# Optimization experiments

Hardware: AMD Instinct MI355X
Metric: run time of the kernel (lower is better)

The kernel has to match this reference:

```python
import math
import jax, jax.numpy as jnp
import numpy as np

B, S, H, NH = 2, 2048, 1024, 16
HD = H // NH


def setup_inputs() -> dict:
    key = jax.random.key(0)
    k1, k2, k3 = jax.random.split(key, 3)
    scale = 1.0 / math.sqrt(H)
    return {
        "hidden_states": jax.random.normal(k1, (B, S, H), dtype=jnp.float32),
        "attention_mask": jnp.ones((B, 1, S, S), dtype=jnp.float32),
        "qkv_w": jax.random.normal(k2, (3 * H, H), dtype=jnp.float32) * scale,
        "qkv_b": jnp.zeros((3 * H,), dtype=jnp.float32),
        "dense_w": jax.random.normal(k3, (H, H), dtype=jnp.float32) * scale,
        "dense_b": jnp.zeros((H,), dtype=jnp.float32),
    }


def reference(hidden_states, attention_mask, qkv_w, qkv_b, dense_w, dense_b):
    # qkv projection: torch Linear y = x @ W^T + b
    mixed = hidden_states @ qkv_w.T + qkv_b            # [B,S,3H]
    mixed = mixed.reshape(B, S, NH, 3 * HD).transpose(0, 2, 1, 3)  # [B,NH,S,3HD]
    q, k, v = jnp.split(mixed, 3, axis=-1)             # each [B,NH,S,HD]
    scores = jnp.einsum("bhqd,bhkd->bhqk", q, k) / math.sqrt(HD)
    scores = scores * attention_mask - 10000.0 * (1.0 - attention_mask)
    probs = jax.nn.softmax(scores, axis=-1)            # dropout p=0 -> identity
    ctx = jnp.einsum("bhqk,bhkd->bhqd", probs, v)      # [B,NH,S,HD]
    ctx = ctx.transpose(0, 2, 1, 3).reshape(B, S, H)
    out = ctx @ dense_w.T + dense_b                    # output dropout p=0
    return out
```

## Files before the change

### kernel.cpp

```cpp
#include <hip/hip_runtime.h>
#include <hip/hip_bf16.h>
#include <stdint.h>

#define BB 2
#define SS 2048
#define HH 1024
#define NHH 16
#define HDD 64
#define MM (BB*SS)
#define N1 (3*HH)
#define NT (SS/64)
#define LOG2E 1.44269504f

using bf16 = __hip_bfloat16;
typedef __attribute__((ext_vector_type(8))) short bf16x8;
typedef __attribute__((ext_vector_type(4))) float f32x4;

__device__ inline unsigned short f2bfu(float f) {
  union { bf16 h; unsigned short u; } c;
  c.h = __float2bfloat16(f);
  return c.u;
}

__device__ inline unsigned int cvtpk(float lo, float hi) {
  unsigned int r;
  asm("v_cvt_pk_bf16_f32 %0, %1, %2" : "=v"(r) : "v"(lo), "v"(hi));
  return r;
}

__device__ inline void load_lds16(const void* g, void* l) {
  __builtin_amdgcn_global_load_lds(
      (const __attribute__((address_space(1))) void*)g,
      (__attribute__((address_space(3))) void*)l, 16, 0, 0);
}

__device__ inline f32x4 mfma16(bf16x8 a, bf16x8 b, f32x4 c) {
  return __builtin_amdgcn_mfma_f32_16x16x32_bf16(a, b, c, 0, 0, 0);
}

__global__ __launch_bounds__(256) void prep_kernel(const float* __restrict__ mask,
                                                   unsigned char* __restrict__ flags,
                                                   const float* __restrict__ a,
                                                   unsigned short* __restrict__ ao, int na4,
                                                   const float* __restrict__ bsrc,
                                                   unsigned short* __restrict__ bo, int nb4,
                                                   const float* __restrict__ c,
                                                   unsigned short* __restrict__ co, int nc4) {
  if (blockIdx.x < 2048) {
    int t = blockIdx.x;
    int b = t >> 10, qt = (t >> 5) & 31, kt = t & 31;
    const float* mb = mask + ((size_t)b * SS + qt * 64) * SS + kt * 64;
    int row = threadIdx.x >> 2, c0 = (threadIdx.x & 3) * 16;
    int ok = 1;
#pragma unroll
    for (int j = 0; j < 4; ++j) {
      float4 v = *reinterpret_cast<const float4*>(mb + (size_t)row * SS + c0 + j * 4);
      ok &= (v.x == 1.f) & (v.y == 1.f) & (v.z == 1.f) & (v.w == 1.f);
    }
    ok = __all(ok);
    __shared__ int s[4];
    if ((threadIdx.x & 63) == 0) s[threadIdx.x >> 6] = ok;
    __syncthreads();
    if (threadIdx.x == 0) flags[t] = (unsigned char)(s[0] & s[1] & s[2] & s[3]);
    return;
  }
  int total = na4 + nb4 + nc4;
  int nblk = gridDim.x - 2048;
  int st = nblk * blockDim.x;
  for (int i = (blockIdx.x - 2048) * blockDim.x + threadIdx.x; i < total; i += st) {
    const float* in; unsigned short* out; int j = i;
    if (j < na4) { in = a; out = ao; }
    else if (j < na4 + nb4) { j -= na4; in = bsrc; out = bo; }
    else { j -= na4 + nb4; in = c; out = co; }
    float4 v = reinterpret_cast<const float4*>(in)[j];
    ushort4 o;
    o.x = f2bfu(v.x); o.y = f2bfu(v.y); o.z = f2bfu(v.z); o.w = f2bfu(v.w);
    reinterpret_cast<ushort4*>(out)[j] = o;
  }
}

__global__ __launch_bounds__(256) void vtrans_kernel(const unsigned short* __restrict__ mixed,
                                                     unsigned short* __restrict__ vT) {
  __shared__ unsigned short t[64 * 72];
  const int st = blockIdx.x, bh = blockIdx.y;
  const int b = bh >> 4, h = bh & 15;
  const int r = threadIdx.x >> 2, c0 = (threadIdx.x & 3) * 16;

  const unsigned short* src = mixed + ((size_t)(b * SS) + st * 64) * N1 + h * 192 + 128;
  union { bf16x8 v; unsigned short u[8]; } A, B;
  A.v = *reinterpret_cast<const bf16x8*>(src + (size_t)r * N1 + c0);
  B.v = *reinterpret_cast<const bf16x8*>(src + (size_t)r * N1 + c0 + 8);
#pragma unroll
  for (int j = 0; j < 8; ++j) t[(c0 + j) * 72 + r] = A.u[j];
#pragma unroll
  for (int j = 0; j < 8; ++j) t[(c0 + 8 + j) * 72 + r] = B.u[j];
  __syncthreads();

  unsigned short* dst = vT + ((size_t)bh * HDD + r) * SS + st * 64 + c0;
  bf16x8 o0 = *reinterpret_cast<const bf16x8*>(&t[r * 72 + c0]);
  bf16x8 o1 = *reinterpret_cast<const bf16x8*>(&t[r * 72 + c0 + 8]);
  *reinterpret_cast<bf16x8*>(dst) = o0;
  *reinterpret_cast<bf16x8*>(dst + 8) = o1;
}

template <bool OUT_BF16>
__global__ __launch_bounds__(256) void gemm_bt(const unsigned short* __restrict__ A,
                                               const unsigned short* __restrict__ Bt,
                                               const float* __restrict__ bias,
                                               void* __restrict__ Cv,
                                               int Ndim, int Kdim) {
  __shared__ __align__(16) unsigned short As[128 * 64];
  __shared__ __align__(16) unsigned short Bs[128 * 64];

  const int tid = threadIdx.x;
  const int wave = tid >> 6, lane = tid & 63;
  const int m0 = blockIdx.x * 128;
  const int n0 = blockIdx.y * 128;
  const int wm = (wave >> 1) * 64, wn = (wave & 1) * 64;
  const int lrow = lane & 15;
  const int g = lane >> 4;
  const int r4 = (lane >> 4) * 4;
  const int x0 = (g ^ (lrow & 7)) << 3;
  const int x1 = ((g + 4) ^ (lrow & 7)) << 3;

  f32x4 acc[4][4];
  const f32x4 z = {0.f, 0.f, 0.f, 0.f};
  for (int i = 0; i < 4; ++i)
    for (int j = 0; j < 4; ++j) acc[i][j] = z;

  for (int k0 = 0; k0 < Kdim; k0 += 64) {
#pragma unroll
    for (int it = 0; it < 4; ++it) {
      int idx = it * 256 + tid;
      int row = idx >> 3, seg = idx & 7;
      int sw = (seg ^ (row & 7)) << 3;
      load_lds16(A + (size_t)(m0 + row) * Kdim + k0 + sw, &As[row * 64 + seg * 8]);
      load_lds16(Bt + (size_t)(n0 + row) * Kdim + k0 + sw, &Bs[row * 64 + seg * 8]);
    }
    __syncthreads();

    bf16x8 af[4], bfr[4];
#pragma unroll
    for (int i = 0; i < 4; ++i)
      af[i] = *reinterpret_cast<const bf16x8*>(&As[(wm + i * 16 + lrow) * 64 + x0]);
#pragma unroll
    for (int j = 0; j < 4; ++j)
      bfr[j] = *reinterpret_cast<const bf16x8*>(&Bs[(wn + j * 16 + lrow) * 64 + x0]);
#pragma unroll
    for (int i = 0; i < 4; ++i)
#pragma unroll
      for (int j = 0; j < 4; ++j)
        acc[i][j] = mfma16(af[i], bfr[j], acc[i][j]);
#pragma unroll
    for (int i = 0; i < 4; ++i)
      af[i] = *reinterpret_cast<const bf16x8*>(&As[(wm + i * 16 + lrow) * 64 + x1]);
#pragma unroll
    for (int j = 0; j < 4; ++j)
      bfr[j] = *reinterpret_cast<const bf16x8*>(&Bs[(wn + j * 16 + lrow) * 64 + x1]);
#pragma unroll
    for (int i = 0; i < 4; ++i)
#pragma unroll
      for (int j = 0; j < 4; ++j)
        acc[i][j] = mfma16(af[i], bfr[j], acc[i][j]);
    __syncthreads();
  }

#pragma unroll
  for (int i = 0; i < 4; ++i) {
#pragma unroll
    for (int j = 0; j < 4; ++j) {
      int col = n0 + wn + j * 16 + lrow;
      float bv = bias[col];
#pragma unroll
      for (int r = 0; r < 4; ++r) {
        int row = m0 + wm + i * 16 + r4 + r;
        float v = acc[i][j][r] + bv;
        if (OUT_BF16) {
          ((unsigned short*)Cv)[(size_t)row * Ndim + col] = f2bfu(v);
        } else {
          ((float*)Cv)[(size_t)row * Ndim + col] = v;
        }
      }
    }
  }
}

__global__ __launch_bounds__(256, 4) void attn_kernel(const unsigned short* __restrict__ mixed,
                                                      const unsigned short* __restrict__ vT,
                                                      const float* __restrict__ mask,
                                                      const unsigned char* __restrict__ flags,
                                                      unsigned short* __restrict__ ctx) {
  __shared__ __align__(16) unsigned short Ks[2][64 * 64];
  __shared__ __align__(16) unsigned short Vt[2][64 * 64];
  __shared__ __align__(16) unsigned short QP[64 * 64];

  const int tid = threadIdx.x, wave = tid >> 6, lane = tid & 63;
  const int ql = lane & 15;
  const int g = lane >> 4;
  const int q0 = blockIdx.x * 64;
  const int bh = blockIdx.y;
  const int b = bh / NHH, hh = bh % NHH;

  const unsigned short* qbase = mixed + (size_t)(b * SS) * N1 + hh * 192;
  const unsigned short* kbase = qbase + 64;
  const unsigned short* vtbase = vT + ((size_t)(b * NHH + hh) * HDD) * SS;
  const float* mbase = mask + (size_t)b * SS * SS;
  const unsigned char* fl = flags + ((size_t)b * 32 + blockIdx.x) * 32;

  const int srow = tid >> 3, sseg = tid & 7;
  const int swst = (sseg ^ (srow & 7)) << 3;

  load_lds16(qbase + (size_t)(q0 + srow) * N1 + swst, &QP[srow * 64 + sseg * 8]);
  load_lds16(qbase + (size_t)(q0 + 32 + srow) * N1 + swst, &QP[(32 + srow) * 64 + sseg * 8]);
  load_lds16(kbase + (size_t)srow * N1 + swst, &Ks[0][srow * 64 + sseg * 8]);
  load_lds16(kbase + (size_t)(32 + srow) * N1 + swst, &Ks[0][(32 + srow) * 64 + sseg * 8]);
  load_lds16(vtbase + (size_t)srow * SS + swst, &Vt[0][srow * 64 + sseg * 8]);
  load_lds16(vtbase + (size_t)(32 + srow) * SS + swst, &Vt[0][(32 + srow) * 64 + sseg * 8]);
  __syncthreads();

  const int qrow = wave * 16 + ql;
  const bf16x8 qf0 = *reinterpret_cast<const bf16x8*>(
      &QP[qrow * 64 + ((g ^ (qrow & 7)) << 3)]);
  const bf16x8 qf1 = *reinterpret_cast<const bf16x8*>(
      &QP[qrow * 64 + (((g + 4) ^ (qrow & 7)) << 3)]);
  __syncthreads();

  const int s0 = (g ^ (ql & 7)) << 3;
  const int s1 = ((g + 4) ^ (ql & 7)) << 3;
  const unsigned short* KrA = &Ks[0][ql * 64 + s0];
  const unsigned short* KrB = &Ks[0][ql * 64 + s1];
  const unsigned short* VrA = &Vt[0][ql * 64 + s0];
  const unsigned short* VrB = &Vt[0][ql * 64 + s1];
  unsigned short* Ps = &QP[wave * 1024];
  const int X = (ql & 7) << 3;
  unsigned short* Pw0 = &Ps[ql * 64 + ((4 * g) ^ X)];
  unsigned short* Pw1 = &Ps[ql * 64 + ((16 + 4 * g) ^ X)];
  unsigned short* Pw2 = &Ps[ql * 64 + ((32 + 4 * g) ^ X)];
  unsigned short* Pw3 = &Ps[ql * 64 + ((48 + 4 * g) ^ X)];
  const unsigned short* Pr0 = &Ps[ql * 64 + ((8 * g) ^ X)];
  const unsigned short* Pr1 = &Ps[ql * 64 + ((32 + 8 * g) ^ X)];

  const unsigned short* kpre = kbase + (size_t)(64 + srow) * N1 + swst;
  const unsigned short* vpre = vtbase + (size_t)srow * SS + 64 + swst;

  f32x4 oacc[4];
  const f32x4 z = {0.f, 0.f, 0.f, 0.f};
  for (int fd = 0; fd < 4; ++fd) oacc[fd] = z;
  float lsum = 0.f;
  const float C2 = 0.125f * LOG2E;

#define TILE_BODY(CUR_, KT_, HAVENEXT_)                                         \
  {                                                                             \
    const int kt_ = (KT_);                                                      \
    if (HAVENEXT_) {                                                            \
      load_lds16(kpre, &Ks[(CUR_)^1][srow * 64 + sseg * 8]);                    \
      load_lds16(kpre + 32 * N1, &Ks[(CUR_)^1][(32 + srow) * 64 + sseg * 8]);   \
      load_lds16(vpre, &Vt[(CUR_)^1][srow * 64 + sseg * 8]);                    \
      load_lds16(vpre + 32 * SS, &Vt[(CUR_)^1][(32 + srow) * 64 + sseg * 8]);   \
    }                                                                           \
    kpre += 64 * N1; vpre += 64;                                                \
    f32x4 sacc[4];                                                              \
    __builtin_amdgcn_s_setprio(1);                                              \
    _Pragma("unroll")                                                           \
    for (int n = 0; n < 4; ++n) {                                               \
      bf16x8 k0 = *reinterpret_cast<const bf16x8*>(KrA + (CUR_)*4096 + n*1024); \
      bf16x8 k1 = *reinterpret_cast<const bf16x8*>(KrB + (CUR_)*4096 + n*1024); \
      sacc[n] = mfma16(k0, qf0, z);                                             \
      sacc[n] = mfma16(k1, qf1, sacc[n]);                                       \
    }                                                                           \
    __builtin_amdgcn_s_setprio(0);                                              \
              \
    bf16x8 bv00 = *reinterpret_cast<const bf16x8*>(VrA + (CUR_)*4096 + 0*1024); \
    bf16x8 bv10 = *reinterpret_cast<const bf16x8*>(VrB + (CUR_)*4096 + 0*1024); \
    bf16x8 bv01 = *reinterpret_cast<const bf16x8*>(VrA + (CUR_)*4096 + 1*1024); \
    bf16x8 bv11 = *reinterpret_cast<const bf16x8*>(VrB + (CUR_)*4096 + 1*1024); \
    bf16x8 bv02 = *reinterpret_cast<const bf16x8*>(VrA + (CUR_)*4096 + 2*1024); \
    bf16x8 bv12 = *reinterpret_cast<const bf16x8*>(VrB + (CUR_)*4096 + 2*1024); \
    bf16x8 bv03 = *reinterpret_cast<const bf16x8*>(VrA + (CUR_)*4096 + 3*1024); \
    bf16x8 bv13 = *reinterpret_cast<const bf16x8*>(VrB + (CUR_)*4096 + 3*1024); \
    const bool allones = fl[kt_] != 0;                                          \
    float pv[4][4];                                                             \
    if (allones) {                                                              \
      _Pragma("unroll")                                                         \
      for (int n = 0; n < 4; ++n)                                               \
        _Pragma("unroll")                                                       \
        for (int r = 0; r < 4; ++r)                                             \
          pv[n][r] = exp2f(sacc[n][r] * C2);                                    \
    } else {                                                                    \
      int qq = q0 + wave * 16 + ql;                                             \
      _Pragma("unroll")                                                         \
      for (int n = 0; n < 4; ++n)                                               \
        _Pragma("unroll")                                                       \
        for (int r = 0; r < 4; ++r) {                                           \
          int kk = kt_ * 64 + 16 * n + 4 * g + r;                               \
          float mv = mbase[(size_t)qq * SS + kk];                               \
          float s = sacc[n][r] * 0.125f;                                        \
          pv[n][r] = exp2f((s * mv - 10000.f * (1.f - mv)) * LOG2E);            \
        }                                                                       \
    }                                                                           \
    { uint2 w; w.x = cvtpk(pv[0][0], pv[0][1]); w.y = cvtpk(pv[0][2], pv[0][3]);\
      *reinterpret_cast<uint2*>(Pw0) = w; }                                     \
    { uint2 w; w.x = cvtpk(pv[1][0], pv[1][1]); w.y = cvtpk(pv[1][2], pv[1][3]);\
      *reinterpret_cast<uint2*>(Pw1) = w; }                                     \
    { uint2 w; w.x = cvtpk(pv[2][0], pv[2][1]); w.y = cvtpk(pv[2][2], pv[2][3]);\
      *reinterpret_cast<uint2*>(Pw2) = w; }                                     \
    { uint2 w; w.x = cvtpk(pv[3][0], pv[3][1]); w.y = cvtpk(pv[3][2], pv[3][3]);\
      *reinterpret_cast<uint2*>(Pw3) = w; }                                     \
                    \
    {                                                                           \
      float t00 = (pv[0][0] + pv[0][1]) + (pv[0][2] + pv[0][3]);                \
      float t01 = (pv[1][0] + pv[1][1]) + (pv[1][2] + pv[1][3]);                \
      float t10 = (pv[2][0] + pv[2][1]) + (pv[2][2] + pv[2][3]);                \
      float t11 = (pv[3][0] + pv[3][1]) + (pv[3][2] + pv[3][3]);                \
      lsum += (t00 + t01) + (t10 + t11);                                        \
    }                                                                           \
    bf16x8 pa0 = *reinterpret_cast<const bf16x8*>(Pr0);                         \
    bf16x8 pa1 = *reinterpret_cast<const bf16x8*>(Pr1);                         \
    __builtin_amdgcn_s_setprio(1);                                              \
    oacc[0] = mfma16(pa0, bv00, oacc[0]);                                       \
    oacc[1] = mfma16(pa0, bv01, oacc[1]);                                       \
    oacc[2] = mfma16(pa0, bv02, oacc[2]);                                       \
    oacc[3] = mfma16(pa0, bv03, oacc[3]);                                       \
    oacc[0] = mfma16(pa1, bv10, oacc[0]);                                       \
    oacc[1] = mfma16(pa1, bv11, oacc[1]);                                       \
    oacc[2] = mfma16(pa1, bv12, oacc[2]);                                       \
    oacc[3] = mfma16(pa1, bv13, oacc[3]);                                       \
    __builtin_amdgcn_s_setprio(0);                                              \
    __syncthreads();                                                            \
  }

  for (int kt = 0; kt < NT; kt += 2) {
    TILE_BODY(0, kt, true)
    TILE_BODY(1, kt + 1, (kt + 2 < NT))
  }
#undef TILE_BODY

  float lrun = lsum;
  lrun += __shfl_xor(lrun, 16, 64);
  lrun += __shfl_xor(lrun, 32, 64);
  float invl = 1.f / lrun;
#pragma unroll
  for (int r = 0; r < 4; ++r) {
    float inv = __shfl(invl, g * 4 + r, 64);
    int qq = q0 + wave * 16 + g * 4 + r;
    unsigned short* cp = ctx + (size_t)(b * SS + qq) * HH + hh * HDD;
#pragma unroll
    for (int fd = 0; fd < 4; ++fd)
      cp[fd * 16 + ql] = f2bfu(oacc[fd][r] * inv);
  }
}

extern "C" void kernel_launch(void* const* d_in, const int* in_sizes, int n_in,
                              void* d_out, int out_size, void* d_ws, size_t ws_size,
                              hipStream_t stream) {
  const float* hs      = (const float*)d_in[0];
  const float* mask    = (const float*)d_in[1];
  const float* qkv_w   = (const float*)d_in[2];
  const float* qkv_b   = (const float*)d_in[3];
  const float* dense_w = (const float*)d_in[4];
  const float* dense_b = (const float*)d_in[5];
  float* out = (float*)d_out;

  char* ws = (char*)d_ws;
  unsigned short* hs_b     = (unsigned short*)(ws);
  unsigned short* qkvw_b   = (unsigned short*)(ws + 8388608);
  unsigned short* densew_b = (unsigned short*)(ws + 14680064);
  unsigned short* mixed_b  = (unsigned short*)(ws + 16777216);
  unsigned short* ctx_b    = (unsigned short*)(ws + 41943040);
  unsigned char*  flags    = (unsigned char*)(ws + 50331648);
  unsigned short* vT_b     = (unsigned short*)(ws + 50335744);

  prep_kernel<<<4096, 256, 0, stream>>>(mask, flags,
                                        hs, hs_b, (MM * HH) / 4,
                                        qkv_w, qkvw_b, (N1 * HH) / 4,
                                        dense_w, densew_b, (HH * HH) / 4);

  gemm_bt<true><<<dim3(MM / 128, N1 / 128), 256, 0, stream>>>(
      hs_b, qkvw_b, qkv_b, mixed_b, N1, HH);

  vtrans_kernel<<<dim3(SS / 64, BB * NHH), 256, 0, stream>>>(mixed_b, vT_b);

  attn_kernel<<<dim3(SS / 64, BB * NHH), 256, 0, stream>>>(
      mixed_b, vT_b, mask, flags, ctx_b);

  gemm_bt<false><<<dim3(MM / 128, HH / 128), 256, 0, stream>>>(
      ctx_b, densew_b, dense_b, out, HH, HH);
}
```

Before: 146.8 us.

## Split KV tiles across wave pairs with 32-row waves and LDS merge

Each wave now handles 32 query rows instead of 16. Each K and V fragment read from LDS therefore feeds two MFMA chains, which halves LDS fragment traffic per FLOP. The two wave pairs alternate over KV tiles: one pair computes while the next tile is staged. At the end, pair 1's partial outputs and row sums go through LDS and are added into pair 0's results before normalization. In exchange, register pressure roughly doubles, only half the waves in a block compute at any moment, and a final reduction step is added.

```diff
diff --git a/kernel.cpp b/kernel.cpp
--- a/kernel.cpp
+++ b/kernel.cpp
@@ -197,6 +197,8 @@
   const int tid = threadIdx.x, wave = tid >> 6, lane = tid & 63;
   const int ql = lane & 15;
   const int g = lane >> 4;
+  const int pair = wave >> 1;
+  const int rb = (wave & 1) * 32;
   const int q0 = blockIdx.x * 64;
   const int bh = blockIdx.y;
   const int b = bh / NHH, hh = bh % NHH;
@@ -218,11 +220,11 @@
   load_lds16(vtbase + (size_t)(32 + srow) * SS + swst, &Vt[0][(32 + srow) * 64 + sseg * 8]);
   __syncthreads();
 
-  const int qrow = wave * 16 + ql;
-  const bf16x8 qf0 = *reinterpret_cast<const bf16x8*>(
-      &QP[qrow * 64 + ((g ^ (qrow & 7)) << 3)]);
-  const bf16x8 qf1 = *reinterpret_cast<const bf16x8*>(
-      &QP[qrow * 64 + (((g + 4) ^ (qrow & 7)) << 3)]);
+  const int qrA = rb + ql, qrB = rb + 16 + ql;
+  const bf16x8 qfA0 = *reinterpret_cast<const bf16x8*>(&QP[qrA * 64 + ((g ^ (qrA & 7)) << 3)]);
+  const bf16x8 qfA1 = *reinterpret_cast<const bf16x8*>(&QP[qrA * 64 + (((g + 4) ^ (qrA & 7)) << 3)]);
+  const bf16x8 qfB0 = *reinterpret_cast<const bf16x8*>(&QP[qrB * 64 + ((g ^ (qrB & 7)) << 3)]);
+  const bf16x8 qfB1 = *reinterpret_cast<const bf16x8*>(&QP[qrB * 64 + (((g + 4) ^ (qrB & 7)) << 3)]);
   __syncthreads();
 
   const int s0 = (g ^ (ql & 7)) << 3;
@@ -243,110 +245,167 @@
   const unsigned short* kpre = kbase + (size_t)(64 + srow) * N1 + swst;
   const unsigned short* vpre = vtbase + (size_t)srow * SS + 64 + swst;
 
-  f32x4 oacc[4];
+  f32x4 oaccA[4], oaccB[4];
   const f32x4 z = {0.f, 0.f, 0.f, 0.f};
-  for (int fd = 0; fd < 4; ++fd) oacc[fd] = z;
-  float lsum = 0.f;
+  for (int fd = 0; fd < 4; ++fd) { oaccA[fd] = z; oaccB[fd] = z; }
+  float lsumA = 0.f, lsumB = 0.f;
   const float C2 = 0.125f * LOG2E;
 
-#define TILE_BODY(CUR_, KT_, HAVENEXT_)                                         \
+#define STAGE(NXT_)                                                             \
+  {                                                                             \
+    load_lds16(kpre, &Ks[NXT_][srow * 64 + sseg * 8]);                          \
+    load_lds16(kpre + 32 * N1, &Ks[NXT_][(32 + srow) * 64 + sseg * 8]);         \
+    load_lds16(vpre, &Vt[NXT_][srow * 64 + sseg * 8]);                          \
+    load_lds16(vpre + 32 * SS, &Vt[NXT_][(32 + srow) * 64 + sseg * 8]);         \
+    kpre += 64 * N1; vpre += 64;                                                \
+  }
+
+#define COMPUTE(CUR_, KT_)                                                      \
   {                                                                             \
     const int kt_ = (KT_);                                                      \
-    if (HAVENEXT_) {                                                            \
-      load_lds16(kpre, &Ks[(CUR_)^1][srow * 64 + sseg * 8]);                    \
-      load_lds16(kpre + 32 * N1, &Ks[(CUR_)^1][(32 + srow) * 64 + sseg * 8]);   \
-      load_lds16(vpre, &Vt[(CUR_)^1][srow * 64 + sseg * 8]);                    \
-      load_lds16(vpre + 32 * SS, &Vt[(CUR_)^1][(32 + srow) * 64 + sseg * 8]);   \
-    }                                                                           \
-    kpre += 64 * N1; vpre += 64;                                                \
-    f32x4 sacc[4];                                                              \
+    f32x4 saccA[4], saccB[4];                                                   \
     __builtin_amdgcn_s_setprio(1);                                              \
     _Pragma("unroll")                                                           \
     for (int n = 0; n < 4; ++n) {                                               \
       bf16x8 k0 = *reinterpret_cast<const bf16x8*>(KrA + (CUR_)*4096 + n*1024); \
       bf16x8 k1 = *reinterpret_cast<const bf16x8*>(KrB + (CUR_)*4096 + n*1024); \
-      sacc[n] = mfma16(k0, qf0, z);                                             \
-      sacc[n] = mfma16(k1, qf1, sacc[n]);                                       \
+      saccA[n] = mfma16(k0, qfA0, z);                                           \
+      saccA[n] = mfma16(k1, qfA1, saccA[n]);                                    \
+      saccB[n] = mfma16(k0, qfB0, z);                                           \
+      saccB[n] = mfma16(k1, qfB1, saccB[n]);                                    \
     }                                                                           \
     __builtin_amdgcn_s_setprio(0);                                              \
-              \
-    bf16x8 bv00 = *reinterpret_cast<const bf16x8*>(VrA + (CUR_)*4096 + 0*1024); \
-    bf16x8 bv10 = *reinterpret_cast<const bf16x8*>(VrB + (CUR_)*4096 + 0*1024); \
-    bf16x8 bv01 = *reinterpret_cast<const bf16x8*>(VrA + (CUR_)*4096 + 1*1024); \
-    bf16x8 bv11 = *reinterpret_cast<const bf16x8*>(VrB + (CUR_)*4096 + 1*1024); \
-    bf16x8 bv02 = *reinterpret_cast<const bf16x8*>(VrA + (CUR_)*4096 + 2*1024); \
-    bf16x8 bv12 = *reinterpret_cast<const bf16x8*>(VrB + (CUR_)*4096 + 2*1024); \
-    bf16x8 bv03 = *reinterpret_cast<const bf16x8*>(VrA + (CUR_)*4096 + 3*1024); \
-    bf16x8 bv13 = *reinterpret_cast<const bf16x8*>(VrB + (CUR_)*4096 + 3*1024); \
     const bool allones = fl[kt_] != 0;                                          \
-    float pv[4][4];                                                             \
+    float pvA[4][4], pvB[4][4];                                                 \
     if (allones) {                                                              \
       _Pragma("unroll")                                                         \
       for (int n = 0; n < 4; ++n)                                               \
         _Pragma("unroll")                                                       \
-        for (int r = 0; r < 4; ++r)                                             \
-          pv[n][r] = exp2f(sacc[n][r] * C2);                                    \
+        for (int r = 0; r < 4; ++r) {                                           \
+          pvA[n][r] = exp2f(saccA[n][r] * C2);                                  \
+          pvB[n][r] = exp2f(saccB[n][r] * C2);                                  \
+        }                                                                       \
     } else {                                                                    \
-      int qq = q0 + wave * 16 + ql;                                             \
+      int qqA = q0 + rb + ql;                                                   \
       _Pragma("unroll")                                                         \
       for (int n = 0; n < 4; ++n)                                               \
         _Pragma("unroll")                                                       \
         for (int r = 0; r < 4; ++r) {                                           \
           int kk = kt_ * 64 + 16 * n + 4 * g + r;                               \
-          float mv = mbase[(size_t)qq * SS + kk];                               \
-          float s = sacc[n][r] * 0.125f;                                        \
-          pv[n][r] = exp2f((s * mv - 10000.f * (1.f - mv)) * LOG2E);            \
+          float mvA = mbase[(size_t)qqA * SS + kk];                             \
+          float mvB = mbase[(size_t)(qqA + 16) * SS + kk];                      \
+          float sA = saccA[n][r] * 0.125f;                                      \
+          float sB = saccB[n][r] * 0.125f;                                      \
+          pvA[n][r] = exp2f((sA * mvA - 10000.f * (1.f - mvA)) * LOG2E);        \
+          pvB[n][r] = exp2f((sB * mvB - 10000.f * (1.f - mvB)) * LOG2E);        \
         }                                                                       \
     }                                                                           \
-    { uint2 w; w.x = cvtpk(pv[0][0], pv[0][1]); w.y = cvtpk(pv[0][2], pv[0][3]);\
+    {                                                                           \
+      float tA0 = (pvA[0][0] + pvA[0][1]) + (pvA[0][2] + pvA[0][3]);            \
+      float tA1 = (pvA[1][0] + pvA[1][1]) + (pvA[1][2] + pvA[1][3]);            \
+      float tA2 = (pvA[2][0] + pvA[2][1]) + (pvA[2][2] + pvA[2][3]);            \
+      float tA3 = (pvA[3][0] + pvA[3][1]) + (pvA[3][2] + pvA[3][3]);            \
+      lsumA += (tA0 + tA1) + (tA2 + tA3);                                       \
+      float tB0 = (pvB[0][0] + pvB[0][1]) + (pvB[0][2] + pvB[0][3]);            \
+      float tB1 = (pvB[1][0] + pvB[1][1]) + (pvB[1][2] + pvB[1][3]);            \
+      float tB2 = (pvB[2][0] + pvB[2][1]) + (pvB[2][2] + pvB[2][3]);            \
+      float tB3 = (pvB[3][0] + pvB[3][1]) + (pvB[3][2] + pvB[3][3]);            \
+      lsumB += (tB0 + tB1) + (tB2 + tB3);                                       \
+    }                                                                           \
+         \
+    { uint2 w; w.x = cvtpk(pvA[0][0], pvA[0][1]); w.y = cvtpk(pvA[0][2], pvA[0][3]); \
       *reinterpret_cast<uint2*>(Pw0) = w; }                                     \
-    { uint2 w; w.x = cvtpk(pv[1][0], pv[1][1]); w.y = cvtpk(pv[1][2], pv[1][3]);\
+    { uint2 w; w.x = cvtpk(pvA[1][0], pvA[1][1]); w.y = cvtpk(pvA[1][2], pvA[1][3]); \
       *reinterpret_cast<uint2*>(Pw1) = w; }                                     \
-    { uint2 w; w.x = cvtpk(pv[2][0], pv[2][1]); w.y = cvtpk(pv[2][2], pv[2][3]);\
+    { uint2 w; w.x = cvtpk(pvA[2][0], pvA[2][1]); w.y = cvtpk(pvA[2][2], pvA[2][3]); \
       *reinterpret_cast<uint2*>(Pw2) = w; }                                     \
-    { uint2 w; w.x = cvtpk(pv[3][0], pv[3][1]); w.y = cvtpk(pv[3][2], pv[3][3]);\
+    { uint2 w; w.x = cvtpk(pvA[3][0], pvA[3][1]); w.y = cvtpk(pvA[3][2], pvA[3][3]); \
       *reinterpret_cast<uint2*>(Pw3) = w; }                                     \
-                    \
-    {                                                                           \
-      float t00 = (pv[0][0] + pv[0][1]) + (pv[0][2] + pv[0][3]);                \
-      float t01 = (pv[1][0] + pv[1][1]) + (pv[1][2] + pv[1][3]);                \
-      float t10 = (pv[2][0] + pv[2][1]) + (pv[2][2] + pv[2][3]);                \
-      float t11 = (pv[3][0] + pv[3][1]) + (pv[3][2] + pv[3][3]);                \
-      lsum += (t00 + t01) + (t10 + t11);                                        \
+    bf16x8 paA0 = *reinterpret_cast<const bf16x8*>(Pr0);                        \
+    bf16x8 paA1 = *reinterpret_cast<const bf16x8*>(Pr1);                        \
+    { uint2 w; w.x = cvtpk(pvB[0][0], pvB[0][1]); w.y = cvtpk(pvB[0][2], pvB[0][3]); \
+      *reinterpret_cast<uint2*>(Pw0) = w; }                                     \
+    { uint2 w; w.x = cvtpk(pvB[1][0], pvB[1][1]); w.y = cvtpk(pvB[1][2], pvB[1][3]); \
+      *reinterpret_cast<uint2*>(Pw1) = w; }                                     \
+    { uint2 w; w.x = cvtpk(pvB[2][0], pvB[2][1]); w.y = cvtpk(pvB[2][2], pvB[2][3]); \
+      *reinterpret_cast<uint2*>(Pw2) = w; }                                     \
+    { uint2 w; w.x = cvtpk(pvB[3][0], pvB[3][1]); w.y = cvtpk(pvB[3][2], pvB[3][3]); \
+      *reinterpret_cast<uint2*>(Pw3) = w; }                                     \
+    bf16x8 paB0 = *reinterpret_cast<const bf16x8*>(Pr0);                        \
+    bf16x8 paB1 = *reinterpret_cast<const bf16x8*>(Pr1);                        \
+                        \
+    __builtin_amdgcn_s_setprio(1);                                              \
+    _Pragma("unroll")                                                           \
+    for (int fd = 0; fd < 4; ++fd) {                                            \
+      bf16x8 bv0 = *reinterpret_cast<const bf16x8*>(VrA + (CUR_)*4096 + fd*1024); \
+      bf16x8 bv1 = *reinterpret_cast<const bf16x8*>(VrB + (CUR_)*4096 + fd*1024); \
+      oaccA[fd] = mfma16(paA0, bv0, oaccA[fd]);                                 \
+      oaccA[fd] = mfma16(paA1, bv1, oaccA[fd]);                                 \
+      oaccB[fd] = mfma16(paB0, bv0, oaccB[fd]);                                 \
+      oaccB[fd] = mfma16(paB1, bv1, oaccB[fd]);                                 \
     }                                                                           \
-    bf16x8 pa0 = *reinterpret_cast<const bf16x8*>(Pr0);                         \
-    bf16x8 pa1 = *reinterpret_cast<const bf16x8*>(Pr1);                         \
-    __builtin_amdgcn_s_setprio(1);                                              \
-    oacc[0] = mfma16(pa0, bv00, oacc[0]);                                       \
-    oacc[1] = mfma16(pa0, bv01, oacc[1]);                                       \
-    oacc[2] = mfma16(pa0, bv02, oacc[2]);                                       \
-    oacc[3] = mfma16(pa0, bv03, oacc[3]);                                       \
-    oacc[0] = mfma16(pa1, bv10, oacc[0]);                                       \
-    oacc[1] = mfma16(pa1, bv11, oacc[1]);                                       \
-    oacc[2] = mfma16(pa1, bv12, oacc[2]);                                       \
-    oacc[3] = mfma16(pa1, bv13, oacc[3]);                                       \
     __builtin_amdgcn_s_setprio(0);                                              \
-    __syncthreads();                                                            \
   }
 
   for (int kt = 0; kt < NT; kt += 2) {
-    TILE_BODY(0, kt, true)
-    TILE_BODY(1, kt + 1, (kt + 2 < NT))
-  }
-#undef TILE_BODY
-
-  float lrun = lsum;
-  lrun += __shfl_xor(lrun, 16, 64);
-  lrun += __shfl_xor(lrun, 32, 64);
-  float invl = 1.f / lrun;
-#pragma unroll
-  for (int r = 0; r < 4; ++r) {
-    float inv = __shfl(invl, g * 4 + r, 64);
-    int qq = q0 + wave * 16 + g * 4 + r;
-    unsigned short* cp = ctx + (size_t)(b * SS + qq) * HH + hh * HDD;
-#pragma unroll
-    for (int fd = 0; fd < 4; ++fd)
-      cp[fd * 16 + ql] = f2bfu(oacc[fd][r] * inv);
+    STAGE(1)
+    if (pair == 0) COMPUTE(0, kt)
+    __syncthreads();
+    if (kt + 2 < NT) STAGE(0)
+    if (pair == 1) COMPUTE(1, kt + 1)
+    __syncthreads();
+  }
+#undef STAGE
+#undef COMPUTE
+
+  lsumA += __shfl_xor(lsumA, 16, 64);
+  lsumA += __shfl_xor(lsumA, 32, 64);
+  lsumB += __shfl_xor(lsumB, 16, 64);
+  lsumB += __shfl_xor(lsumB, 32, 64);
+
+  float* Osh = reinterpret_cast<float*>(&Ks[0][0]);
+  float* Lsh = reinterpret_cast<float*>(&Vt[0][0]);
+  if (pair == 1) {
+#pragma unroll
+    for (int r = 0; r < 4; ++r) {
+      int rowA = rb + g * 4 + r, rowB = rb + 16 + g * 4 + r;
+#pragma unroll
+      for (int fd = 0; fd < 4; ++fd) {
+        Osh[rowA * 64 + fd * 16 + ql] = oaccA[fd][r];
+        Osh[rowB * 64 + fd * 16 + ql] = oaccB[fd][r];
+      }
+    }
+    Lsh[rb + ql] = lsumA;
+    Lsh[rb + 16 + ql] = lsumB;
+  }
+  __syncthreads();
+  if (pair == 0) {
+#pragma unroll
+    for (int r = 0; r < 4; ++r) {
+      int rowA = rb + g * 4 + r, rowB = rb + 16 + g * 4 + r;
+#pragma unroll
+      for (int fd = 0; fd < 4; ++fd) {
+        oaccA[fd][r] += Osh[rowA * 64 + fd * 16 + ql];
+        oaccB[fd][r] += Osh[rowB * 64 + fd * 16 + ql];
+      }
+    }
+    float lA = lsumA + Lsh[rb + ql];
+    float lB = lsumB + Lsh[rb + 16 + ql];
+    float invA = 1.f / lA;
+    float invB = 1.f / lB;
+#pragma unroll
+    for (int r = 0; r < 4; ++r) {
+      float iA = __shfl(invA, g * 4 + r, 64);
+      float iB = __shfl(invB, g * 4 + r, 64);
+      int qqA = q0 + rb + g * 4 + r;
+      unsigned short* cpA = ctx + (size_t)(b * SS + qqA) * HH + hh * HDD;
+      unsigned short* cpB = ctx + (size_t)(b * SS + qqA + 16) * HH + hh * HDD;
+#pragma unroll
+      for (int fd = 0; fd < 4; ++fd) {
+        cpA[fd * 16 + ql] = f2bfu(oaccA[fd][r] * iA);
+        cpB[fd * 16 + ql] = f2bfu(oaccB[fd][r] * iB);
+      }
+    }
   }
 }
 
```

Result: slower. 184.6 us (+25.7%).

## Split QKV GEMM into QK and V GEMMs writing transposed V directly

Applied to the files above, without the earlier changes.

Replaces the single QKV projection GEMM plus separate V-transpose kernel with two GEMMs. One writes Q/K into a compact per-head buffer, and the other computes V and transposes it through shared memory into the head-major vT layout. This removes the V write and read round trip and one kernel launch. The cost is two launches with a smaller grid each, where gemm_v has only 256 blocks, which may underfill the device.

```diff
diff --git a/kernel.cpp b/kernel.cpp
--- a/kernel.cpp
+++ b/kernel.cpp
@@ -9,6 +9,7 @@
 #define HDD 64
 #define MM (BB*SS)
 #define N1 (3*HH)
+#define QKS 2048
 #define NT (SS/64)
 #define LOG2E 1.44269504f
 
@@ -79,35 +80,179 @@
   }
 }
 
-__global__ __launch_bounds__(256) void vtrans_kernel(const unsigned short* __restrict__ mixed,
-                                                     unsigned short* __restrict__ vT) {
-  __shared__ unsigned short t[64 * 72];
-  const int st = blockIdx.x, bh = blockIdx.y;
-  const int b = bh >> 4, h = bh & 15;
-  const int r = threadIdx.x >> 2, c0 = (threadIdx.x & 3) * 16;
-
-  const unsigned short* src = mixed + ((size_t)(b * SS) + st * 64) * N1 + h * 192 + 128;
-  union { bf16x8 v; unsigned short u[8]; } A, B;
-  A.v = *reinterpret_cast<const bf16x8*>(src + (size_t)r * N1 + c0);
-  B.v = *reinterpret_cast<const bf16x8*>(src + (size_t)r * N1 + c0 + 8);
-#pragma unroll
-  for (int j = 0; j < 8; ++j) t[(c0 + j) * 72 + r] = A.u[j];
-#pragma unroll
-  for (int j = 0; j < 8; ++j) t[(c0 + 8 + j) * 72 + r] = B.u[j];
+__global__ __launch_bounds__(256) void gemm_qk(const unsigned short* __restrict__ A,
+                                               const unsigned short* __restrict__ Bt,
+                                               const float* __restrict__ bias,
+                                               unsigned short* __restrict__ Out) {
+  __shared__ __align__(16) unsigned short As[128 * 64];
+  __shared__ __align__(16) unsigned short Bs[128 * 64];
+
+  const int tid = threadIdx.x;
+  const int wave = tid >> 6, lane = tid & 63;
+  const int m0 = blockIdx.x * 128;
+  const int n0 = blockIdx.y * 128;
+  const int rbase = 192 * blockIdx.y;
+  const int wm = (wave >> 1) * 64, wn = (wave & 1) * 64;
+  const int lrow = lane & 15;
+  const int g = lane >> 4;
+  const int r4 = g * 4;
+  const int x0 = (g ^ (lrow & 7)) << 3;
+  const int x1 = ((g + 4) ^ (lrow & 7)) << 3;
+
+  f32x4 acc[4][4];
+  const f32x4 z = {0.f, 0.f, 0.f, 0.f};
+  for (int i = 0; i < 4; ++i)
+    for (int j = 0; j < 4; ++j) acc[i][j] = z;
+
+  for (int k0 = 0; k0 < HH; k0 += 64) {
+#pragma unroll
+    for (int it = 0; it < 4; ++it) {
+      int idx = it * 256 + tid;
+      int row = idx >> 3, seg = idx & 7;
+      int sw = (seg ^ (row & 7)) << 3;
+      load_lds16(A + (size_t)(m0 + row) * HH + k0 + sw, &As[row * 64 + seg * 8]);
+      load_lds16(Bt + (size_t)(rbase + row) * HH + k0 + sw, &Bs[row * 64 + seg * 8]);
+    }
+    __syncthreads();
+
+    bf16x8 af[4], bfr[4];
+#pragma unroll
+    for (int i = 0; i < 4; ++i)
+      af[i] = *reinterpret_cast<const bf16x8*>(&As[(wm + i * 16 + lrow) * 64 + x0]);
+#pragma unroll
+    for (int j = 0; j < 4; ++j)
+      bfr[j] = *reinterpret_cast<const bf16x8*>(&Bs[(wn + j * 16 + lrow) * 64 + x0]);
+#pragma unroll
+    for (int i = 0; i < 4; ++i)
+#pragma unroll
+      for (int j = 0; j < 4; ++j)
+        acc[i][j] = mfma16(af[i], bfr[j], acc[i][j]);
+#pragma unroll
+    for (int i = 0; i < 4; ++i)
+      af[i] = *reinterpret_cast<const bf16x8*>(&As[(wm + i * 16 + lrow) * 64 + x1]);
+#pragma unroll
+    for (int j = 0; j < 4; ++j)
+      bfr[j] = *reinterpret_cast<const bf16x8*>(&Bs[(wn + j * 16 + lrow) * 64 + x1]);
+#pragma unroll
+    for (int i = 0; i < 4; ++i)
+#pragma unroll
+      for (int j = 0; j < 4; ++j)
+        acc[i][j] = mfma16(af[i], bfr[j], acc[i][j]);
+    __syncthreads();
+  }
+
+#pragma unroll
+  for (int i = 0; i < 4; ++i) {
+#pragma unroll
+    for (int j = 0; j < 4; ++j) {
+      int cl = wn + j * 16 + lrow;
+      float bv = bias[rbase + cl];
+#pragma unroll
+      for (int r = 0; r < 4; ++r) {
+        int row = m0 + wm + i * 16 + r4 + r;
+        Out[(size_t)row * QKS + n0 + cl] = f2bfu(acc[i][j][r] + bv);
+      }
+    }
+  }
+}
+
+__global__ __launch_bounds__(256) void gemm_v(const unsigned short* __restrict__ A,
+                                              const unsigned short* __restrict__ Bt,
+                                              const float* __restrict__ bias,
+                                              unsigned short* __restrict__ vT) {
+  __shared__ __align__(16) unsigned short Sh[2 * 128 * 64];
+  unsigned short* As = Sh;
+  unsigned short* Bs = Sh + 128 * 64;
+
+  const int tid = threadIdx.x;
+  const int wave = tid >> 6, lane = tid & 63;
+  const int m0 = blockIdx.x * 128;
+  const int ny = blockIdx.y;
+  const int wm = (wave >> 1) * 64, wn = (wave & 1) * 64;
+  const int lrow = lane & 15;
+  const int g = lane >> 4;
+  const int r4 = g * 4;
+  const int x0 = (g ^ (lrow & 7)) << 3;
+  const int x1 = ((g + 4) ^ (lrow & 7)) << 3;
+
+  f32x4 acc[4][4];
+  const f32x4 z = {0.f, 0.f, 0.f, 0.f};
+  for (int i = 0; i < 4; ++i)
+    for (int j = 0; j < 4; ++j) acc[i][j] = z;
+
+  for (int k0 = 0; k0 < HH; k0 += 64) {
+#pragma unroll
+    for (int it = 0; it < 4; ++it) {
+      int idx = it * 256 + tid;
+      int row = idx >> 3, seg = idx & 7;
+      int sw = (seg ^ (row & 7)) << 3;
+      int vrow = 192 * (2 * ny + (row >> 6)) + 128 + (row & 63);
+      load_lds16(A + (size_t)(m0 + row) * HH + k0 + sw, &As[row * 64 + seg * 8]);
+      load_lds16(Bt + (size_t)vrow * HH + k0 + sw, &Bs[row * 64 + seg * 8]);
+    }
+    __syncthreads();
+
+    bf16x8 af[4], bfr[4];
+#pragma unroll
+    for (int i = 0; i < 4; ++i)
+      af[i] = *reinterpret_cast<const bf16x8*>(&As[(wm + i * 16 + lrow) * 64 + x0]);
+#pragma unroll
+    for (int j = 0; j < 4; ++j)
+      bfr[j] = *reinterpret_cast<const bf16x8*>(&Bs[(wn + j * 16 + lrow) * 64 + x0]);
+#pragma unroll
+    for (int i = 0; i < 4; ++i)
+#pragma unroll
+      for (int j = 0; j < 4; ++j)
+        acc[i][j] = mfma16(af[i], bfr[j], acc[i][j]);
+#pragma unroll
+    for (int i = 0; i < 4; ++i)
+      af[i] = *reinterpret_cast<const bf16x8*>(&As[(wm + i * 16 + lrow) * 64 + x1]);
+#pragma unroll
+    for (int j = 0; j < 4; ++j)
+      bfr[j] = *reinterpret_cast<const bf16x8*>(&Bs[(wn + j * 16 + lrow) * 64 + x1]);
+#pragma unroll
+    for (int i = 0; i < 4; ++i)
+#pragma unroll
+      for (int j = 0; j < 4; ++j)
+        acc[i][j] = mfma16(af[i], bfr[j], acc[i][j]);
+    __syncthreads();
+  }
+
+  unsigned short* Ct = Sh;
+  const int mb = wm + r4;
+#pragma unroll
+  for (int i = 0; i < 4; ++i) {
+    int m = mb + i * 16;
+    int m8 = m >> 3, mo = m & 7;
+#pragma unroll
+    for (int j = 0; j < 4; ++j) {
+      int cl = wn + j * 16 + lrow;
+      float bv = bias[192 * (2 * ny + (cl >> 6)) + 128 + (cl & 63)];
+      uint2 w;
+      w.x = cvtpk(acc[i][j][0] + bv, acc[i][j][1] + bv);
+      w.y = cvtpk(acc[i][j][2] + bv, acc[i][j][3] + bv);
+      *reinterpret_cast<uint2*>(&Ct[cl * 128 + ((m8 ^ (cl & 7)) << 3) + mo]) = w;
+    }
+  }
   __syncthreads();
 
-  unsigned short* dst = vT + ((size_t)bh * HDD + r) * SS + st * 64 + c0;
-  bf16x8 o0 = *reinterpret_cast<const bf16x8*>(&t[r * 72 + c0]);
-  bf16x8 o1 = *reinterpret_cast<const bf16x8*>(&t[r * 72 + c0 + 8]);
-  *reinterpret_cast<bf16x8*>(dst) = o0;
-  *reinterpret_cast<bf16x8*>(dst + 8) = o1;
-}
-
-template <bool OUT_BF16>
+  const int bb = m0 >> 11;
+  const int s0 = m0 & (SS - 1);
+#pragma unroll
+  for (int it = 0; it < 8; ++it) {
+    int idx = it * 256 + tid;
+    int d = idx >> 4, s8 = idx & 15;
+    bf16x8 v = *reinterpret_cast<const bf16x8*>(&Ct[d * 128 + ((s8 ^ (d & 7)) << 3)]);
+    int head = 2 * ny + (d >> 6), dd = d & 63;
+    *reinterpret_cast<bf16x8*>(
+        vT + ((size_t)(bb * NHH + head) * HDD + dd) * SS + s0 + s8 * 8) = v;
+  }
+}
+
 __global__ __launch_bounds__(256) void gemm_bt(const unsigned short* __restrict__ A,
                                                const unsigned short* __restrict__ Bt,
                                                const float* __restrict__ bias,
-                                               void* __restrict__ Cv,
+                                               float* __restrict__ Cv,
                                                int Ndim, int Kdim) {
   __shared__ __align__(16) unsigned short As[128 * 64];
   __shared__ __align__(16) unsigned short Bs[128 * 64];
@@ -119,7 +264,7 @@
   const int wm = (wave >> 1) * 64, wn = (wave & 1) * 64;
   const int lrow = lane & 15;
   const int g = lane >> 4;
-  const int r4 = (lane >> 4) * 4;
+  const int r4 = g * 4;
   const int x0 = (g ^ (lrow & 7)) << 3;
   const int x1 = ((g + 4) ^ (lrow & 7)) << 3;
 
@@ -174,18 +319,13 @@
 #pragma unroll
       for (int r = 0; r < 4; ++r) {
         int row = m0 + wm + i * 16 + r4 + r;
-        float v = acc[i][j][r] + bv;
-        if (OUT_BF16) {
-          ((unsigned short*)Cv)[(size_t)row * Ndim + col] = f2bfu(v);
-        } else {
-          ((float*)Cv)[(size_t)row * Ndim + col] = v;
-        }
+        Cv[(size_t)row * Ndim + col] = acc[i][j][r] + bv;
       }
     }
   }
 }
 
-__global__ __launch_bounds__(256, 4) void attn_kernel(const unsigned short* __restrict__ mixed,
+__global__ __launch_bounds__(256, 4) void attn_kernel(const unsigned short* __restrict__ qk,
                                                       const unsigned short* __restrict__ vT,
                                                       const float* __restrict__ mask,
                                                       const unsigned char* __restrict__ flags,
@@ -201,7 +341,7 @@
   const int bh = blockIdx.y;
   const int b = bh / NHH, hh = bh % NHH;
 
-  const unsigned short* qbase = mixed + (size_t)(b * SS) * N1 + hh * 192;
+  const unsigned short* qbase = qk + (size_t)(b * SS) * QKS + hh * 128;
   const unsigned short* kbase = qbase + 64;
   const unsigned short* vtbase = vT + ((size_t)(b * NHH + hh) * HDD) * SS;
   const float* mbase = mask + (size_t)b * SS * SS;
@@ -210,10 +350,10 @@
   const int srow = tid >> 3, sseg = tid & 7;
   const int swst = (sseg ^ (srow & 7)) << 3;
 
-  load_lds16(qbase + (size_t)(q0 + srow) * N1 + swst, &QP[srow * 64 + sseg * 8]);
-  load_lds16(qbase + (size_t)(q0 + 32 + srow) * N1 + swst, &QP[(32 + srow) * 64 + sseg * 8]);
-  load_lds16(kbase + (size_t)srow * N1 + swst, &Ks[0][srow * 64 + sseg * 8]);
-  load_lds16(kbase + (size_t)(32 + srow) * N1 + swst, &Ks[0][(32 + srow) * 64 + sseg * 8]);
+  load_lds16(qbase + (size_t)(q0 + srow) * QKS + swst, &QP[srow * 64 + sseg * 8]);
+  load_lds16(qbase + (size_t)(q0 + 32 + srow) * QKS + swst, &QP[(32 + srow) * 64 + sseg * 8]);
+  load_lds16(kbase + (size_t)srow * QKS + swst, &Ks[0][srow * 64 + sseg * 8]);
+  load_lds16(kbase + (size_t)(32 + srow) * QKS + swst, &Ks[0][(32 + srow) * 64 + sseg * 8]);
   load_lds16(vtbase + (size_t)srow * SS + swst, &Vt[0][srow * 64 + sseg * 8]);
   load_lds16(vtbase + (size_t)(32 + srow) * SS + swst, &Vt[0][(32 + srow) * 64 + sseg * 8]);
   __syncthreads();
@@ -240,7 +380,7 @@
   const unsigned short* Pr0 = &Ps[ql * 64 + ((8 * g) ^ X)];
   const unsigned short* Pr1 = &Ps[ql * 64 + ((32 + 8 * g) ^ X)];
 
-  const unsigned short* kpre = kbase + (size_t)(64 + srow) * N1 + swst;
+  const unsigned short* kpre = kbase + (size_t)(64 + srow) * QKS + swst;
   const unsigned short* vpre = vtbase + (size_t)srow * SS + 64 + swst;
 
   f32x4 oacc[4];
@@ -254,11 +394,11 @@
     const int kt_ = (KT_);                                                      \
     if (HAVENEXT_) {                                                            \
       load_lds16(kpre, &Ks[(CUR_)^1][srow * 64 + sseg * 8]);                    \
-      load_lds16(kpre + 32 * N1, &Ks[(CUR_)^1][(32 + srow) * 64 + sseg * 8]);   \
+      load_lds16(kpre + 32 * QKS, &Ks[(CUR_)^1][(32 + srow) * 64 + sseg * 8]);  \
       load_lds16(vpre, &Vt[(CUR_)^1][srow * 64 + sseg * 8]);                    \
       load_lds16(vpre + 32 * SS, &Vt[(CUR_)^1][(32 + srow) * 64 + sseg * 8]);   \
     }                                                                           \
-    kpre += 64 * N1; vpre += 64;                                                \
+    kpre += 64 * QKS; vpre += 64;                                               \
     f32x4 sacc[4];                                                              \
     __builtin_amdgcn_s_setprio(1);                                              \
     _Pragma("unroll")                                                           \
@@ -269,7 +409,6 @@
       sacc[n] = mfma16(k1, qf1, sacc[n]);                                       \
     }                                                                           \
     __builtin_amdgcn_s_setprio(0);                                              \
-              \
     bf16x8 bv00 = *reinterpret_cast<const bf16x8*>(VrA + (CUR_)*4096 + 0*1024); \
     bf16x8 bv10 = *reinterpret_cast<const bf16x8*>(VrB + (CUR_)*4096 + 0*1024); \
     bf16x8 bv01 = *reinterpret_cast<const bf16x8*>(VrA + (CUR_)*4096 + 1*1024); \
@@ -306,7 +445,6 @@
       *reinterpret_cast<uint2*>(Pw2) = w; }                                     \
     { uint2 w; w.x = cvtpk(pv[3][0], pv[3][1]); w.y = cvtpk(pv[3][2], pv[3][3]);\
       *reinterpret_cast<uint2*>(Pw3) = w; }                                     \
-                    \
     {                                                                           \
       float t00 = (pv[0][0] + pv[0][1]) + (pv[0][2] + pv[0][3]);                \
       float t01 = (pv[1][0] + pv[1][1]) + (pv[1][2] + pv[1][3]);                \
@@ -365,7 +503,7 @@
   unsigned short* hs_b     = (unsigned short*)(ws);
   unsigned short* qkvw_b   = (unsigned short*)(ws + 8388608);
   unsigned short* densew_b = (unsigned short*)(ws + 14680064);
-  unsigned short* mixed_b  = (unsigned short*)(ws + 16777216);
+  unsigned short* qk_b     = (unsigned short*)(ws + 16777216);
   unsigned short* ctx_b    = (unsigned short*)(ws + 41943040);
   unsigned char*  flags    = (unsigned char*)(ws + 50331648);
   unsigned short* vT_b     = (unsigned short*)(ws + 50335744);
@@ -375,14 +513,12 @@
                                         qkv_w, qkvw_b, (N1 * HH) / 4,
                                         dense_w, densew_b, (HH * HH) / 4);
 
-  gemm_bt<true><<<dim3(MM / 128, N1 / 128), 256, 0, stream>>>(
-      hs_b, qkvw_b, qkv_b, mixed_b, N1, HH);
-
-  vtrans_kernel<<<dim3(SS / 64, BB * NHH), 256, 0, stream>>>(mixed_b, vT_b);
+  gemm_qk<<<dim3(MM / 128, NHH), 256, 0, stream>>>(hs_b, qkvw_b, qkv_b, qk_b);
+  gemm_v<<<dim3(MM / 128, NHH / 2), 256, 0, stream>>>(hs_b, qkvw_b, qkv_b, vT_b);
 
   attn_kernel<<<dim3(SS / 64, BB * NHH), 256, 0, stream>>>(
-      mixed_b, vT_b, mask, flags, ctx_b);
-
-  gemm_bt<false><<<dim3(MM / 128, HH / 128), 256, 0, stream>>>(
+      qk_b, vT_b, mask, flags, ctx_b);
+
+  gemm_bt<<<dim3(MM / 128, HH / 128), 256, 0, stream>>>(
       ctx_b, densew_b, dense_b, out, HH, HH);
 }
```

Result: slower. 150.5 us (+2.5%).
